# Kernel optimization log

Measured on AMD Instinct MI355X. Metric: run time of the kernel, lower is better.

## Reference

```python
import jax, jax.numpy as jnp
import numpy as np

N, E, G = 50000, 800000, 64
IN, ED = 2, 2
H1, C1 = 16, 8
H2, C2 = 4, 16
D1 = H1 * C1  # 128
D2 = H2 * C2  # 64


def _glorot(key, shape):
    fan_in, fan_out = shape[0], shape[-1]
    lim = jnp.sqrt(6.0 / (fan_in + fan_out))
    return jax.random.uniform(key, shape, jnp.float32, -lim, lim)


def setup_inputs() -> dict:
    key = jax.random.key(0)
    ks = jax.random.split(key, 16)
    x = jax.random.normal(ks[0], (N, IN), jnp.float32)
    edge_attr = jax.random.uniform(ks[1], (E, ED), jnp.float32)
    edge_index = jax.random.randint(ks[2], (2, E), 0, N, jnp.int64)
    batch = jnp.sort(jax.random.randint(ks[3], (N,), 0, G, jnp.int64))
    return {
        'x': x, 'edge_attr': edge_attr,
        'W_l1': _glorot(ks[4], (IN, D1)), 'b_l1': jnp.zeros((D1,), jnp.float32),
        'W_r1': _glorot(ks[5], (IN, D1)), 'b_r1': jnp.zeros((D1,), jnp.float32),
        'W_e1': _glorot(ks[6], (ED, D1)),
        'att1': _glorot(ks[7], (H1, C1)),
        'bias1': jnp.zeros((D1,), jnp.float32),
        'W_l2': _glorot(ks[8], (D1, D2)), 'b_l2': jnp.zeros((D2,), jnp.float32),
        'W_r2': _glorot(ks[9], (D1, D2)), 'b_r2': jnp.zeros((D2,), jnp.float32),
        'W_e2': _glorot(ks[10], (ED, D2)),
        'att2': _glorot(ks[11], (H2, C2)),
        'bias2': jnp.zeros((D2,), jnp.float32),
        'edge_index': edge_index, 'batch': batch,
    }


def _gatv2(x, edge_attr, src, tgt, Wl, bl, Wr, br, We, att, bias, H, C):
    n = x.shape[0]
    xl = (x @ Wl + bl).reshape(n, H, C)          # source transform (lin_l)
    xr = (x @ Wr + br).reshape(n, H, C)          # target transform (lin_r)
    xe = (edge_attr @ We).reshape(-1, H, C)      # edge transform (no bias)
    m = xl[src] + xr[tgt] + xe                   # [E,H,C]
    e = jnp.einsum('ehc,hc->eh', jax.nn.leaky_relu(m, 0.2), att)  # [E,H]
    emax = jax.ops.segment_max(e, tgt, num_segments=n)
    ee = jnp.exp(e - emax[tgt])
    denom = jax.ops.segment_sum(ee, tgt, num_segments=n)
    alpha = ee / denom[tgt]                      # segment softmax over in-edges
    out = jax.ops.segment_sum(alpha[:, :, None] * xl[src], tgt, num_segments=n)
    return out.reshape(n, H * C) + bias


def reference(x, edge_attr, W_l1, b_l1, W_r1, b_r1, W_e1, att1, bias1,
              W_l2, b_l2, W_r2, b_r2, W_e2, att2, bias2, edge_index, batch):
    src, tgt = edge_index[0], edge_index[1]
    h = _gatv2(x, edge_attr, src, tgt, W_l1, b_l1, W_r1, b_r1, W_e1, att1, bias1, H1, C1)
    h = jax.nn.elu(h)  # dropout is identity in eval mode
    h = _gatv2(h, edge_attr, src, tgt, W_l2, b_l2, W_r2, b_r2, W_e2, att2, bias2, H2, C2)
    # global_mean_pool over graphs
    sums = jax.ops.segment_sum(h, batch, num_segments=G)
    cnts = jax.ops.segment_sum(jnp.ones((h.shape[0], 1), h.dtype), batch, num_segments=G)
    return sums / jnp.maximum(cnts, 1.0)
```

## Files before the change

kernel.cpp:

```cpp
#include <hip/hip_runtime.h>
#include <math.h>

#define NBLK 512


template<int CTRL>
__device__ __forceinline__ float dppf(float x) {
    return __int_as_float(__builtin_amdgcn_update_dpp(
        0, __float_as_int(x), CTRL, 0xF, 0xF, true));
}
__device__ __forceinline__ float quadsum(float x) {
    x += dppf<0xB1>(x);
    x += dppf<0x4E>(x);
    return x;
}
__device__ __forceinline__ float sum16(float x) {
    x += dppf<0xB1>(x);
    x += dppf<0x4E>(x);
    x += dppf<0x141>(x);
    x += dppf<0x140>(x);
    return x;
}


__global__ void k_init(float* __restrict__ sums, float* __restrict__ cnt, int gn) {
    int i = blockIdx.x * 256 + threadIdx.x;
    if (i < gn * 64) sums[i] = 0.f;
    if (i < gn) cnt[i] = 0.f;
}


__global__ __launch_bounds__(256) void k_hist(const int* __restrict__ tgt,
                                              int* __restrict__ gh,
                                              int e, int chunk, int nbuck) {
    __shared__ int lh[256];
    int tid = threadIdx.x, blk = blockIdx.x;
    lh[tid] = 0;
    __syncthreads();
    int lo = blk * chunk, hi = min(lo + chunk, e);
    for (int i = lo + tid; i < hi; i += 256)
        atomicAdd(&lh[tgt[i] >> 8], 1);
    __syncthreads();
    if (tid < nbuck) gh[tid * NBLK + blk] = lh[tid];
}


__global__ __launch_bounds__(256) void k_scanA(const int* __restrict__ deg,
                                               int* __restrict__ excl,
                                               int* __restrict__ bsum, int n) {
    int i = blockIdx.x * 256 + threadIdx.x;
    int lane = threadIdx.x & 63, wv = threadIdx.x >> 6;
    int v = (i < n) ? deg[i] : 0;
    int incl = v;
#pragma unroll
    for (int off = 1; off < 64; off <<= 1) {
        int t = __shfl_up(incl, off);
        if (lane >= off) incl += t;
    }
    __shared__ int ws[4];
    if (lane == 63) ws[wv] = incl;
    __syncthreads();
    int prefix = 0;
    for (int k = 0; k < wv; ++k) prefix += ws[k];
    if (i < n) excl[i] = prefix + incl - v;
    if (threadIdx.x == 255) bsum[blockIdx.x] = prefix + incl;
}

__global__ __launch_bounds__(256) void k_scanB(const int* __restrict__ bsum, int* __restrict__ boff,
                                               int nb) {
    __shared__ int ws[4];
    __shared__ int carry_s;
    int lane = threadIdx.x & 63, wv = threadIdx.x >> 6;
    if (threadIdx.x == 0) carry_s = 0;
    __syncthreads();
    for (int base = 0; base < nb; base += 256) {
        int i = base + threadIdx.x;
        int v = (i < nb) ? bsum[i] : 0;
        int incl = v;
#pragma unroll
        for (int off = 1; off < 64; off <<= 1) {
            int t = __shfl_up(incl, off);
            if (lane >= off) incl += t;
        }
        if (lane == 63) ws[wv] = incl;
        __syncthreads();
        int prefix = carry_s;
        for (int k = 0; k < wv; ++k) prefix += ws[k];
        if (i < nb) boff[i] = prefix + incl - v;
        __syncthreads();
        if (threadIdx.x == 255) carry_s = prefix + incl;
        __syncthreads();
    }
}


__global__ __launch_bounds__(256) void k_binplace(const int* __restrict__ src,
                                                  const int* __restrict__ tgt,
                                                  const float* __restrict__ ea,
                                                  const float* __restrict__ x,
                                                  const int* __restrict__ gexcl,
                                                  const int* __restrict__ gboff,
                                                  float4* __restrict__ brec,
                                                  int* __restrict__ bmeta,
                                                  int e, int chunk, int nbuck) {
    __shared__ int loff[256];
    int tid = threadIdx.x, blk = blockIdx.x;
    if (tid < nbuck) {
        int cell = tid * NBLK + blk;
        loff[tid] = gexcl[cell] + gboff[cell >> 8];
    }
    __syncthreads();
    int lo = blk * chunk, hi = min(lo + chunk, e);
    for (int i = lo + tid; i < hi; i += 256) {
        int t = tgt[i], s = src[i];
        float2 ev = ((const float2*)ea)[i];
        float2 xv = *(const float2*)(x + 2 * (size_t)s);
        int dst = atomicAdd(&loff[t >> 8], 1);
        brec[dst] = make_float4(xv.x, xv.y, ev.x, ev.y);
        bmeta[dst] = (s & 0xFFFF) | ((t & 0xFF) << 16);
    }
}


__global__ __launch_bounds__(256) void k_place2(const int* __restrict__ gexcl,
                                                const int* __restrict__ gboff,
                                                const int* __restrict__ bmeta,
                                                const float4* __restrict__ brec,
                                                float4* __restrict__ col_rec,
                                                int* __restrict__ col_src,
                                                int* __restrict__ rowp,
                                                int n, int ntot, int e) {
    __shared__ int hist[256];
    __shared__ int pos[256];
    __shared__ int ws[4];
    int b = blockIdx.x, tid = threadIdx.x;
    int clo = b * NBLK, chi = clo + NBLK;
    int lo = gexcl[clo] + gboff[clo >> 8];
    int hi = (chi >= ntot) ? e : (gexcl[chi] + gboff[chi >> 8]);
    hist[tid] = 0;
    __syncthreads();
    for (int i = lo + tid; i < hi; i += 256)
        atomicAdd(&hist[(bmeta[i] >> 16) & 0xFF], 1);
    __syncthreads();
    int lane = tid & 63, wv = tid >> 6;
    int v = hist[tid];
    int incl = v;
#pragma unroll
    for (int off = 1; off < 64; off <<= 1) {
        int t = __shfl_up(incl, off);
        if (lane >= off) incl += t;
    }
    if (lane == 63) ws[wv] = incl;
    __syncthreads();
    int prefix = 0;
    for (int k = 0; k < wv; ++k) prefix += ws[k];
    int rp = lo + prefix + incl - v;
    int node = b * 256 + tid;
    if (node <= n) rowp[node] = rp;
    if (b == (int)gridDim.x - 1 && tid == 0) rowp[n] = hi;
    pos[tid] = rp;
    __syncthreads();
    for (int i = lo + tid; i < hi; i += 256) {
        int m = bmeta[i];
        float4 r = brec[i];
        int slot = atomicAdd(&pos[(m >> 16) & 0xFF], 1);
        col_rec[slot] = r;
        col_src[slot] = m & 0xFFFF;
    }
}


__global__ __launch_bounds__(256) void k_agg1(
    const float* __restrict__ x,
    const int* __restrict__ rowp,
    const float4* __restrict__ col_rec,
    const float* __restrict__ W_l1, const float* __restrict__ b_l1,
    const float* __restrict__ W_r1, const float* __restrict__ b_r1,
    const float* __restrict__ W_e1,
    const float* __restrict__ att1,
    const float* __restrict__ bias1,
    float* __restrict__ hpost,
    int n)
{
    int wid = (blockIdx.x * blockDim.x + threadIdx.x) >> 6;
    if (wid >= n) return;
    int v = __builtin_amdgcn_readfirstlane(wid);
    int lane = threadIdx.x & 63;
    int f0 = 2 * lane, f1 = 2 * lane + 1;

    float Wl00 = W_l1[f0], Wl10 = W_l1[128 + f0], bl0 = b_l1[f0];
    float Wl01 = W_l1[f1], Wl11 = W_l1[128 + f1], bl1 = b_l1[f1];
    float We00 = W_e1[f0], We10 = W_e1[128 + f0];
    float We01 = W_e1[f1], We11 = W_e1[128 + f1];
    float a0 = att1[f0], a1 = att1[f1];

    float xv0 = x[2 * v], xv1 = x[2 * v + 1];
    float cA = fmaf(xv0, W_r1[f0], fmaf(xv1, W_r1[128 + f0], b_r1[f0])) + bl0;
    float cB = fmaf(xv0, W_r1[f1], fmaf(xv1, W_r1[128 + f1], b_r1[f1])) + bl1;

    float lh = 0.f, px0 = 0.f, px1 = 0.f;
    int rs = rowp[v], re = rowp[v + 1];
    bool b0 = (lane & 1) != 0, b1 = (lane & 2) != 0;

    int cs = rs;
#define E1(K, R) \
    float s##K; { \
        float m0 = fmaf(R.x, Wl00, fmaf(R.y, Wl10, fmaf(R.z, We00, fmaf(R.w, We10, cA)))); \
        float m1 = fmaf(R.x, Wl01, fmaf(R.y, Wl11, fmaf(R.z, We01, fmaf(R.w, We11, cB)))); \
        s##K = quadsum(fmaf(fmaxf(m0, 0.2f * m0), a0, fmaxf(m1, 0.2f * m1) * a1)); \
    }
    for (; cs + 4 <= re; cs += 4) {
        float4 r0 = col_rec[cs + 0];
        float4 r1 = col_rec[cs + 1];
        float4 r2 = col_rec[cs + 2];
        float4 r3 = col_rec[cs + 3];
        E1(0, r0) E1(1, r1) E1(2, r2) E1(3, r3)
        float sel01 = b0 ? s1 : s0;
        float sel23 = b0 ? s3 : s2;
        float smy = b1 ? sel23 : sel01;
        float p = __expf(smy);
        float p0 = dppf<0x00>(p), p1 = dppf<0x55>(p), p2 = dppf<0xAA>(p), p3 = dppf<0xFF>(p);
        lh += (p0 + p1) + (p2 + p3);
        px0 = fmaf(p0, r0.x, px0); px0 = fmaf(p1, r1.x, px0);
        px0 = fmaf(p2, r2.x, px0); px0 = fmaf(p3, r3.x, px0);
        px1 = fmaf(p0, r0.y, px1); px1 = fmaf(p1, r1.y, px1);
        px1 = fmaf(p2, r2.y, px1); px1 = fmaf(p3, r3.y, px1);
    }
#undef E1
    for (; cs < re; ++cs) {
        float4 r = col_rec[cs];
        float m0 = fmaf(r.x, Wl00, fmaf(r.y, Wl10, fmaf(r.z, We00, fmaf(r.w, We10, cA))));
        float m1 = fmaf(r.x, Wl01, fmaf(r.y, Wl11, fmaf(r.z, We01, fmaf(r.w, We11, cB))));
        float s = quadsum(fmaf(fmaxf(m0, 0.2f * m0), a0, fmaxf(m1, 0.2f * m1) * a1));
        float p = __expf(s);
        lh += p;
        px0 = fmaf(p, r.x, px0);
        px1 = fmaf(p, r.y, px1);
    }

    float r0o = 0.f, r1o = 0.f;
    if (re > rs) {
        float inv = 1.f / lh;
        float q0 = px0 * inv, q1 = px1 * inv;
        r0o = fmaf(q0, Wl00, fmaf(q1, Wl10, bl0));
        r1o = fmaf(q0, Wl01, fmaf(q1, Wl11, bl1));
    }
    r0o += bias1[f0]; r1o += bias1[f1];
    r0o = (r0o > 0.f) ? r0o : (__expf(r0o) - 1.f);
    r1o = (r1o > 0.f) ? r1o : (__expf(r1o) - 1.f);
    *(float2*)(hpost + (size_t)v * 128 + f0) = make_float2(r0o, r1o);
}


struct XF2Shared {
    float4 hs[64 * 32];
    float4 ws[128 * 16];
};

__device__ __forceinline__ void xf2_pass(XF2Shared& sm,
                                         const float* __restrict__ W,
                                         const float* __restrict__ b,
                                         float* __restrict__ out,
                                         int v0, int n, int t) {
    __syncthreads();
    {
        const float4* wsrc = (const float4*)W;
#pragma unroll
        for (int i = 0; i < 8; ++i) sm.ws[t + 256 * i] = wsrc[t + 256 * i];
    }
    __syncthreads();

    int lane = t & 63, w = t >> 6;
    int fg = lane & 3, ng = lane >> 2;
    int fq = 4 * w + fg;
    int hsw = ng & 7;

    float acc[4][4];
#pragma unroll
    for (int i = 0; i < 4; ++i)
#pragma unroll
        for (int c = 0; c < 4; ++c) acc[i][c] = 0.f;

    for (int kq = 0; kq < 32; ++kq) {
        float4 w0 = sm.ws[(4 * kq + 0) * 16 + fq];
        float4 w1 = sm.ws[(4 * kq + 1) * 16 + fq];
        float4 w2 = sm.ws[(4 * kq + 2) * 16 + fq];
        float4 w3 = sm.ws[(4 * kq + 3) * 16 + fq];
        int ks = kq ^ hsw;
        float4 h0 = sm.hs[(4 * ng + 0) * 32 + ks];
        float4 h1 = sm.hs[(4 * ng + 1) * 32 + ks];
        float4 h2 = sm.hs[(4 * ng + 2) * 32 + ks];
        float4 h3 = sm.hs[(4 * ng + 3) * 32 + ks];
#pragma unroll
        for (int i = 0; i < 4; ++i) {
            float4 h = (i == 0) ? h0 : (i == 1) ? h1 : (i == 2) ? h2 : h3;
            acc[i][0] += h.x * w0.x; acc[i][1] += h.x * w0.y; acc[i][2] += h.x * w0.z; acc[i][3] += h.x * w0.w;
            acc[i][0] += h.y * w1.x; acc[i][1] += h.y * w1.y; acc[i][2] += h.y * w1.z; acc[i][3] += h.y * w1.w;
            acc[i][0] += h.z * w2.x; acc[i][1] += h.z * w2.y; acc[i][2] += h.z * w2.z; acc[i][3] += h.z * w2.w;
            acc[i][0] += h.w * w3.x; acc[i][1] += h.w * w3.y; acc[i][2] += h.w * w3.z; acc[i][3] += h.w * w3.w;
        }
    }

    float4 bf = ((const float4*)b)[fq];
#pragma unroll
    for (int i = 0; i < 4; ++i) {
        int node = v0 + 4 * ng + i;
        if (node < n) {
            float4 r = make_float4(acc[i][0] + bf.x, acc[i][1] + bf.y,
                                   acc[i][2] + bf.z, acc[i][3] + bf.w);
            *(float4*)(out + (size_t)node * 64 + 4 * fq) = r;
        }
    }
}

__global__ __launch_bounds__(256) void k_transform2(
    const float* __restrict__ hpost,
    const float* __restrict__ W_l2, const float* __restrict__ b_l2,
    const float* __restrict__ W_r2, const float* __restrict__ b_r2,
    float* __restrict__ xl2, float* __restrict__ xr2, int n)
{
    __shared__ XF2Shared sm;
    int t = threadIdx.x;
    int v0 = blockIdx.x * 64;
    {
        int node = t >> 2, sub = t & 3;
        int sw = (node >> 2) & 7;
        bool valid = (v0 + node) < n;
        const float4* src = (const float4*)(hpost + (size_t)(v0 + node) * 128);
#pragma unroll
        for (int i = 0; i < 8; ++i) {
            int kq = sub + 4 * i;
            float4 val = valid ? src[kq] : make_float4(0.f, 0.f, 0.f, 0.f);
            sm.hs[node * 32 + (kq ^ sw)] = val;
        }
    }
    xf2_pass(sm, W_l2, b_l2, xl2, v0, n, t);
    xf2_pass(sm, W_r2, b_r2, xr2, v0, n, t);
}


__global__ __launch_bounds__(256) void k_agg2(
    const float* __restrict__ xl2,
    const float* __restrict__ xr2,
    const int* __restrict__ rowp,
    const int* __restrict__ col_src,
    const float4* __restrict__ col_rec,
    const float* __restrict__ W_e2,
    const float* __restrict__ att2,
    const float* __restrict__ bias2,
    float* __restrict__ h2,
    int n)
{
    int wid = (blockIdx.x * blockDim.x + threadIdx.x) >> 6;
    if (wid >= n) return;
    int v = __builtin_amdgcn_readfirstlane(wid);
    int lane = threadIdx.x & 63;
    float We0 = W_e2[lane], We1 = W_e2[64 + lane];
    float a = att2[lane];
    float xr = xr2[(size_t)v * 64 + lane];
    float lh = 0.f, acc = 0.f;
    int rs = rowp[v], re = rowp[v + 1];
    const float2* eap = (const float2*)col_rec;
    bool b0 = (lane & 1) != 0, b1 = (lane & 2) != 0;

    int cs = rs;
#define E2(K, EV, XL) \
    float s##K; { \
        float m = fmaf(EV.x, We0, fmaf(EV.y, We1, XL + xr)); \
        s##K = sum16(fmaxf(m, 0.2f * m) * a); \
    }
    for (; cs + 4 <= re; cs += 4) {
        int u0 = col_src[cs], u1 = col_src[cs + 1], u2 = col_src[cs + 2], u3 = col_src[cs + 3];
        float2 e0 = eap[2 * cs + 1], e1 = eap[2 * cs + 3];
        float2 e2 = eap[2 * cs + 5], e3 = eap[2 * cs + 7];
        float xl0 = xl2[(size_t)u0 * 64 + lane];
        float xl1 = xl2[(size_t)u1 * 64 + lane];
        float xl2_ = xl2[(size_t)u2 * 64 + lane];
        float xl3 = xl2[(size_t)u3 * 64 + lane];
        E2(0, e0, xl0) E2(1, e1, xl1) E2(2, e2, xl2_) E2(3, e3, xl3)
        float sel01 = b0 ? s1 : s0;
        float sel23 = b0 ? s3 : s2;
        float smy = b1 ? sel23 : sel01;
        float p = __expf(smy);
        float p0 = dppf<0x00>(p), p1 = dppf<0x55>(p), p2 = dppf<0xAA>(p), p3 = dppf<0xFF>(p);
        lh += (p0 + p1) + (p2 + p3);
        acc = fmaf(p0, xl0, acc); acc = fmaf(p1, xl1, acc);
        acc = fmaf(p2, xl2_, acc); acc = fmaf(p3, xl3, acc);
    }
#undef E2
    for (; cs < re; ++cs) {
        int u = col_src[cs];
        float2 ev = eap[2 * cs + 1];
        float xl = xl2[(size_t)u * 64 + lane];
        float m = fmaf(ev.x, We0, fmaf(ev.y, We1, xl + xr));
        float s = sum16(fmaxf(m, 0.2f * m) * a);
        float p = __expf(s);
        lh += p;
        acc = fmaf(p, xl, acc);
    }
    float r = (re > rs) ? acc / lh : 0.f;
    h2[(size_t)v * 64 + lane] = r + bias2[lane];
}


__global__ __launch_bounds__(256) void k_pool2(const float* __restrict__ h2,
                                               const int* __restrict__ batch,
                                               float* __restrict__ sums, float* __restrict__ cnt,
                                               int n, int chunk) {
    int w = (blockIdx.x * blockDim.x + threadIdx.x) >> 6;
    int lane = threadIdx.x & 63;
    int start = w * chunk;
    if (start >= n) return;
    int end = min(n, start + chunk);
    int g = batch[start];
    float acc = 0.f;
    int c = 0;
    for (int v = start; v < end; ++v) {
        int bg = batch[v];
        if (bg != g) {
            atomicAdd(&sums[g * 64 + lane], acc);
            if (lane == 0) atomicAdd(&cnt[g], (float)c);
            acc = 0.f; c = 0; g = bg;
        }
        acc += h2[(size_t)v * 64 + lane];
        ++c;
    }
    atomicAdd(&sums[g * 64 + lane], acc);
    if (lane == 0) atomicAdd(&cnt[g], (float)c);
}

__global__ void k_final(const float* __restrict__ sums, const float* __restrict__ cnt,
                        float* __restrict__ out, int g) {
    int i = blockIdx.x * blockDim.x + threadIdx.x;
    if (i < g * 64) out[i] = sums[i] / fmaxf(cnt[i >> 6], 1.f);
}


extern "C" void kernel_launch(void* const* d_in, const int* in_sizes, int n_in,
                              void* d_out, int out_size, void* d_ws, size_t ws_size,
                              hipStream_t stream) {
    const float* x     = (const float*)d_in[0];
    const float* ea    = (const float*)d_in[1];
    const float* W_l1  = (const float*)d_in[2];
    const float* b_l1  = (const float*)d_in[3];
    const float* W_r1  = (const float*)d_in[4];
    const float* b_r1  = (const float*)d_in[5];
    const float* W_e1  = (const float*)d_in[6];
    const float* att1  = (const float*)d_in[7];
    const float* bias1 = (const float*)d_in[8];
    const float* W_l2  = (const float*)d_in[9];
    const float* b_l2  = (const float*)d_in[10];
    const float* W_r2  = (const float*)d_in[11];
    const float* b_r2  = (const float*)d_in[12];
    const float* W_e2  = (const float*)d_in[13];
    const float* att2  = (const float*)d_in[14];
    const float* bias2 = (const float*)d_in[15];
    const int* eidx    = (const int*)d_in[16];
    const int* batch   = (const int*)d_in[17];

    int n = in_sizes[0] / 2;
    int e = in_sizes[16] / 2;
    int g = out_size / 64;
    const int* srcI = eidx;
    const int* tgtI = eidx + e;
    int nb = (n + 255) / 256;
    int ntot = nb * NBLK;
    int nb2 = (ntot + 255) / 256;
    int chunk = (e + NBLK - 1) / NBLK;

    char* w = (char*)d_ws;
    size_t off = 0;
    auto take = [&](size_t bytes) -> char* {
        size_t a = (off + 255) & ~(size_t)255;
        off = a + bytes;
        return w + a;
    };
    char*   reg1    = take((size_t)n * 128 * 4);
    float4* brec    = (float4*)reg1;
    float*  hpost   = (float*)reg1;
    float*  h2      = hpost;
    char*   reg2    = take((size_t)n * 64 * 4);
    int*    bmeta   = (int*)reg2;
    float*  xl2     = (float*)reg2;

    float*  xr2     = (float*)take((size_t)n * 64 * 4);
    float4* col_rec = (float4*)take((size_t)e * 16);
    int*    col_src = (int*)take((size_t)e * 4);
    int*    rowp    = (int*)take((size_t)(n + 1) * 4);
    int*    gh      = (int*)take((size_t)ntot * 4);
    int*    gexcl   = (int*)take((size_t)(ntot + 1) * 4);
    int*    gbsum   = (int*)take((size_t)nb2 * 4);
    int*    gboff   = (int*)take((size_t)nb2 * 4);
    float*  sums    = (float*)take((size_t)g * 64 * 4);
    float*  cnt     = (float*)take((size_t)g * 4);

    k_init<<<(g * 64 + 255) / 256, 256, 0, stream>>>(sums, cnt, g);

    k_hist<<<NBLK, 256, 0, stream>>>(tgtI, gh, e, chunk, nb);
    k_scanA<<<nb2, 256, 0, stream>>>(gh, gexcl, gbsum, ntot);
    k_scanB<<<1, 256, 0, stream>>>(gbsum, gboff, nb2);
    k_binplace<<<NBLK, 256, 0, stream>>>(srcI, tgtI, ea, x, gexcl, gboff, brec, bmeta,
                                         e, chunk, nb);
    k_place2<<<nb, 256, 0, stream>>>(gexcl, gboff, bmeta, brec, col_rec, col_src, rowp,
                                     n, ntot, e);

    int nwaveblocks = (n * 64 + 255) / 256;
    k_agg1<<<nwaveblocks, 256, 0, stream>>>(x, rowp, col_rec,
                                            W_l1, b_l1, W_r1, b_r1, W_e1, att1, bias1,
                                            hpost, n);
    int ntiles = (n + 63) / 64;
    k_transform2<<<ntiles, 256, 0, stream>>>(hpost, W_l2, b_l2, W_r2, b_r2, xl2, xr2, n);
    k_agg2<<<nwaveblocks, 256, 0, stream>>>(xl2, xr2, rowp, col_src, col_rec,
                                            W_e2, att2, bias2, h2, n);

    int pool_waves = 1024;
    int pool_chunk = (n + pool_waves - 1) / pool_waves;
    k_pool2<<<pool_waves / 4, 256, 0, stream>>>(h2, batch, sums, cnt, n, pool_chunk);
    k_final<<<(g * 64 + 255) / 256, 256, 0, stream>>>(sums, cnt, (float*)d_out, g);
}
```

Baseline: 178.2 us.

## Store per-head layer-1 aggregates and halve node buckets for CSR build

Layer-1 aggregation now writes only the two normalized per-head aggregates plus a has-edges flag per node, instead of the full 128-wide post-ELU hidden row. The lin_l projection, biases and ELU are recomputed inside the layer-2 transform kernel, which cuts the intermediate traffic to about a quarter. Separately, CSR construction buckets 128 nodes instead of 256. That gives twice as many k_place2 blocks and smaller per-bucket histograms, at the cost of more histogram cells and scan work.

```diff
diff --git a/kernel.cpp b/kernel.cpp
--- a/kernel.cpp
+++ b/kernel.cpp
@@ -2,6 +2,8 @@
 #include <math.h>
 
 #define NBLK 512
+#define BSHIFT 7
+#define BMASK 127
 
 
 template<int CTRL>
@@ -33,15 +35,15 @@
 __global__ __launch_bounds__(256) void k_hist(const int* __restrict__ tgt,
                                               int* __restrict__ gh,
                                               int e, int chunk, int nbuck) {
-    __shared__ int lh[256];
+    __shared__ int lh[512];
     int tid = threadIdx.x, blk = blockIdx.x;
-    lh[tid] = 0;
+    for (int j = tid; j < nbuck; j += 256) lh[j] = 0;
     __syncthreads();
     int lo = blk * chunk, hi = min(lo + chunk, e);
     for (int i = lo + tid; i < hi; i += 256)
-        atomicAdd(&lh[tgt[i] >> 8], 1);
-    __syncthreads();
-    if (tid < nbuck) gh[tid * NBLK + blk] = lh[tid];
+        atomicAdd(&lh[tgt[i] >> BSHIFT], 1);
+    __syncthreads();
+    for (int j = tid; j < nbuck; j += 256) gh[j * NBLK + blk] = lh[j];
 }
 
 
@@ -103,11 +105,11 @@
                                                   float4* __restrict__ brec,
                                                   int* __restrict__ bmeta,
                                                   int e, int chunk, int nbuck) {
-    __shared__ int loff[256];
+    __shared__ int loff[512];
     int tid = threadIdx.x, blk = blockIdx.x;
-    if (tid < nbuck) {
-        int cell = tid * NBLK + blk;
-        loff[tid] = gexcl[cell] + gboff[cell >> 8];
+    for (int j = tid; j < nbuck; j += 256) {
+        int cell = j * NBLK + blk;
+        loff[j] = gexcl[cell] + gboff[cell >> 8];
     }
     __syncthreads();
     int lo = blk * chunk, hi = min(lo + chunk, e);
@@ -115,9 +117,9 @@
         int t = tgt[i], s = src[i];
         float2 ev = ((const float2*)ea)[i];
         float2 xv = *(const float2*)(x + 2 * (size_t)s);
-        int dst = atomicAdd(&loff[t >> 8], 1);
+        int dst = atomicAdd(&loff[t >> BSHIFT], 1);
         brec[dst] = make_float4(xv.x, xv.y, ev.x, ev.y);
-        bmeta[dst] = (s & 0xFFFF) | ((t & 0xFF) << 16);
+        bmeta[dst] = (s & 0xFFFF) | ((t & BMASK) << 16);
     }
 }
 
@@ -140,7 +142,7 @@
     hist[tid] = 0;
     __syncthreads();
     for (int i = lo + tid; i < hi; i += 256)
-        atomicAdd(&hist[(bmeta[i] >> 16) & 0xFF], 1);
+        atomicAdd(&hist[(bmeta[i] >> 16) & BMASK], 1);
     __syncthreads();
     int lane = tid & 63, wv = tid >> 6;
     int v = hist[tid];
@@ -155,15 +157,15 @@
     int prefix = 0;
     for (int k = 0; k < wv; ++k) prefix += ws[k];
     int rp = lo + prefix + incl - v;
-    int node = b * 256 + tid;
-    if (node <= n) rowp[node] = rp;
+    int node = b * 128 + tid;
+    if (tid < 128 && node <= n) rowp[node] = rp;
     if (b == (int)gridDim.x - 1 && tid == 0) rowp[n] = hi;
     pos[tid] = rp;
     __syncthreads();
     for (int i = lo + tid; i < hi; i += 256) {
         int m = bmeta[i];
         float4 r = brec[i];
-        int slot = atomicAdd(&pos[(m >> 16) & 0xFF], 1);
+        int slot = atomicAdd(&pos[(m >> 16) & BMASK], 1);
         col_rec[slot] = r;
         col_src[slot] = m & 0xFFFF;
     }
@@ -178,8 +180,8 @@
     const float* __restrict__ W_r1, const float* __restrict__ b_r1,
     const float* __restrict__ W_e1,
     const float* __restrict__ att1,
-    const float* __restrict__ bias1,
-    float* __restrict__ hpost,
+    float2* __restrict__ qbuf,
+    int* __restrict__ flags,
     int n)
 {
     int wid = (blockIdx.x * blockDim.x + threadIdx.x) >> 6;
@@ -188,15 +190,15 @@
     int lane = threadIdx.x & 63;
     int f0 = 2 * lane, f1 = 2 * lane + 1;
 
-    float Wl00 = W_l1[f0], Wl10 = W_l1[128 + f0], bl0 = b_l1[f0];
-    float Wl01 = W_l1[f1], Wl11 = W_l1[128 + f1], bl1 = b_l1[f1];
+    float Wl00 = W_l1[f0], Wl10 = W_l1[128 + f0];
+    float Wl01 = W_l1[f1], Wl11 = W_l1[128 + f1];
     float We00 = W_e1[f0], We10 = W_e1[128 + f0];
     float We01 = W_e1[f1], We11 = W_e1[128 + f1];
     float a0 = att1[f0], a1 = att1[f1];
 
     float xv0 = x[2 * v], xv1 = x[2 * v + 1];
-    float cA = fmaf(xv0, W_r1[f0], fmaf(xv1, W_r1[128 + f0], b_r1[f0])) + bl0;
-    float cB = fmaf(xv0, W_r1[f1], fmaf(xv1, W_r1[128 + f1], b_r1[f1])) + bl1;
+    float cA = fmaf(xv0, W_r1[f0], fmaf(xv1, W_r1[128 + f0], b_r1[f0])) + b_l1[f0];
+    float cB = fmaf(xv0, W_r1[f1], fmaf(xv1, W_r1[128 + f1], b_r1[f1])) + b_l1[f1];
 
     float lh = 0.f, px0 = 0.f, px1 = 0.f;
     int rs = rowp[v], re = rowp[v + 1];
@@ -238,17 +240,10 @@
         px1 = fmaf(p, r.y, px1);
     }
 
-    float r0o = 0.f, r1o = 0.f;
-    if (re > rs) {
-        float inv = 1.f / lh;
-        float q0 = px0 * inv, q1 = px1 * inv;
-        r0o = fmaf(q0, Wl00, fmaf(q1, Wl10, bl0));
-        r1o = fmaf(q0, Wl01, fmaf(q1, Wl11, bl1));
-    }
-    r0o += bias1[f0]; r1o += bias1[f1];
-    r0o = (r0o > 0.f) ? r0o : (__expf(r0o) - 1.f);
-    r1o = (r1o > 0.f) ? r1o : (__expf(r1o) - 1.f);
-    *(float2*)(hpost + (size_t)v * 128 + f0) = make_float2(r0o, r1o);
+    float inv = (re > rs) ? 1.f / lh : 0.f;
+    if ((lane & 3) == 0)
+        qbuf[(size_t)v * 16 + (lane >> 2)] = make_float2(px0 * inv, px1 * inv);
+    if (lane == 0) flags[v] = (re > rs) ? 1 : 0;
 }
 
 
@@ -313,8 +308,14 @@
     }
 }
 
+__device__ __forceinline__ float elu1(float v) {
+    return (v > 0.f) ? v : (__expf(v) - 1.f);
+}
+
 __global__ __launch_bounds__(256) void k_transform2(
-    const float* __restrict__ hpost,
+    const float2* __restrict__ qbuf, const int* __restrict__ flags,
+    const float* __restrict__ W_l1, const float* __restrict__ b_l1,
+    const float* __restrict__ bias1,
     const float* __restrict__ W_l2, const float* __restrict__ b_l2,
     const float* __restrict__ W_r2, const float* __restrict__ b_r2,
     float* __restrict__ xl2, float* __restrict__ xr2, int n)
@@ -325,12 +326,26 @@
     {
         int node = t >> 2, sub = t & 3;
         int sw = (node >> 2) & 7;
-        bool valid = (v0 + node) < n;
-        const float4* src = (const float4*)(hpost + (size_t)(v0 + node) * 128);
+        int gn = v0 + node;
+        bool valid = gn < n;
+        int fl = valid ? flags[gn] : 0;
+        const float4* wl0 = (const float4*)W_l1;
+        const float4* wl1 = (const float4*)(W_l1 + 128);
+        const float4* blp = (const float4*)b_l1;
+        const float4* bip = (const float4*)bias1;
+        float flf = (float)fl;
 #pragma unroll
         for (int i = 0; i < 8; ++i) {
             int kq = sub + 4 * i;
-            float4 val = valid ? src[kq] : make_float4(0.f, 0.f, 0.f, 0.f);
+            float2 q = valid ? qbuf[(size_t)gn * 16 + (kq >> 1)] : make_float2(0.f, 0.f);
+            float4 w0 = wl0[kq], w1 = wl1[kq];
+            float4 bl = blp[kq], bi = bip[kq];
+            float4 val;
+            val.x = elu1(fmaf(q.x, w0.x, fmaf(q.y, w1.x, fmaf(flf, bl.x, bi.x))));
+            val.y = elu1(fmaf(q.x, w0.y, fmaf(q.y, w1.y, fmaf(flf, bl.y, bi.y))));
+            val.z = elu1(fmaf(q.x, w0.z, fmaf(q.y, w1.z, fmaf(flf, bl.z, bi.z))));
+            val.w = elu1(fmaf(q.x, w0.w, fmaf(q.y, w1.w, fmaf(flf, bl.w, bi.w))));
+            if (!valid) val = make_float4(0.f, 0.f, 0.f, 0.f);
             sm.hs[node * 32 + (kq ^ sw)] = val;
         }
     }
@@ -463,7 +478,7 @@
     int g = out_size / 64;
     const int* srcI = eidx;
     const int* tgtI = eidx + e;
-    int nb = (n + 255) / 256;
+    int nb = (n + 127) / 128;
     int ntot = nb * NBLK;
     int nb2 = (ntot + 255) / 256;
     int chunk = (e + NBLK - 1) / NBLK;
@@ -475,10 +490,9 @@
         off = a + bytes;
         return w + a;
     };
-    char*   reg1    = take((size_t)n * 128 * 4);
+    char*   reg1    = take((size_t)e * 16);
     float4* brec    = (float4*)reg1;
-    float*  hpost   = (float*)reg1;
-    float*  h2      = hpost;
+    float*  h2      = (float*)reg1;
     char*   reg2    = take((size_t)n * 64 * 4);
     int*    bmeta   = (int*)reg2;
     float*  xl2     = (float*)reg2;
@@ -487,6 +501,8 @@
     float4* col_rec = (float4*)take((size_t)e * 16);
     int*    col_src = (int*)take((size_t)e * 4);
     int*    rowp    = (int*)take((size_t)(n + 1) * 4);
+    float2* qbuf    = (float2*)take((size_t)n * 16 * 8);
+    int*    flags   = (int*)take((size_t)n * 4);
     int*    gh      = (int*)take((size_t)ntot * 4);
     int*    gexcl   = (int*)take((size_t)(ntot + 1) * 4);
     int*    gbsum   = (int*)take((size_t)nb2 * 4);
@@ -506,10 +522,11 @@
 
     int nwaveblocks = (n * 64 + 255) / 256;
     k_agg1<<<nwaveblocks, 256, 0, stream>>>(x, rowp, col_rec,
-                                            W_l1, b_l1, W_r1, b_r1, W_e1, att1, bias1,
-                                            hpost, n);
+                                            W_l1, b_l1, W_r1, b_r1, W_e1, att1,
+                                            qbuf, flags, n);
     int ntiles = (n + 63) / 64;
-    k_transform2<<<ntiles, 256, 0, stream>>>(hpost, W_l2, b_l2, W_r2, b_r2, xl2, xr2, n);
+    k_transform2<<<ntiles, 256, 0, stream>>>(qbuf, flags, W_l1, b_l1, bias1,
+                                             W_l2, b_l2, W_r2, b_r2, xl2, xr2, n);
     k_agg2<<<nwaveblocks, 256, 0, stream>>>(xl2, xr2, rowp, col_src, col_rec,
                                             W_e2, att2, bias2, h2, n);
 
```

After: 180.9 us. No clear change (+1.5%).
